# Performance work log

Measured on AMD Instinct MI355X. Metric: run time of the kernel, lower is better.

The kernel has to match this reference:

```python
import jax, jax.numpy as jnp
import numpy as np

B, N, K, C = 4, 4096, 32, 192  # batch, npoint, nsample, channels (C % 6 == 0)
EPS = 1e-5


def setup_inputs() -> dict:
    key = jax.random.key(0)
    ks = jax.random.split(key, 8)
    p = jax.random.normal(ks[0], (B, N, 3), jnp.float32)
    x = jax.random.normal(ks[1], (B, C, N), jnp.float32)
    idx = jax.random.randint(ks[2], (B, N, K), 0, N)  # ball-query neighbor ids
    W = jax.random.normal(ks[3], (C, C + 3), jnp.float32) * 0.05  # 1x1 conv weight
    gamma = 1.0 + 0.1 * jax.random.normal(ks[4], (C,), jnp.float32)
    beta = 0.1 * jax.random.normal(ks[5], (C,), jnp.float32)
    rmean = 0.1 * jax.random.normal(ks[6], (C,), jnp.float32)
    rvar = jax.random.uniform(ks[7], (C,), jnp.float32) + 0.5  # positive running var
    return dict(p=p, x=x, idx=idx, W=W, gamma=gamma, beta=beta, rmean=rmean, rvar=rvar)


def reference(p, x, idx, W, gamma, beta, rmean, rvar):
    # --- grouper: gather neighbors, relative coords ---
    pn = jax.vmap(lambda pp, ii: pp[ii])(p, idx)            # [B,N,K,3]
    dp = jnp.transpose(pn - p[:, :, None, :], (0, 3, 1, 2))  # [B,3,N,K]
    xj = jax.vmap(lambda xx, ii: xx[:, ii])(x, idx)          # [B,C,N,K]
    # --- PosPool sin/cos positional embedding fused with features ---
    feat_dim = C // 6
    dim_mat = jnp.power(500.0, jnp.arange(feat_dim, dtype=jnp.float32) / feat_dim)
    div = (50.0 * dp)[..., None] / dim_mat                   # [B,3,N,K,fd]
    pe = jnp.concatenate([jnp.sin(div), jnp.cos(div)], axis=-1)  # [B,3,N,K,2fd]
    pe = jnp.transpose(pe, (0, 1, 4, 2, 3)).reshape(B, C, N, K)  # [B,C,N,K]
    agg = xj * pe + pe
    # --- dp_fj concat -> 1x1 conv -> BN(eval) -> ReLU ---
    h = jnp.concatenate([dp, agg], axis=1)                   # [B,C+3,N,K]
    y = jnp.einsum('oc,bcnk->bonk', W, h)                    # [B,C,N,K]
    inv = gamma / jnp.sqrt(rvar + EPS)
    y = y * inv[:, None, None] + (beta - rmean * inv)[:, None, None]
    y = jax.nn.relu(y)
    # --- max reduction over neighbors ---
    return jnp.max(y, axis=-1)                               # [B,C,N]
```

## Files before the change

### kernel.cpp

```cpp
#include <hip/hip_runtime.h>
#include <math.h>

#define B_   4
#define N_   4096
#define K_   32
#define C_   192
#define CH_  195
#define KPAD 224
#define NKT  7
#define NNT  4
#define NPAIR (B_ * N_ / 2)
#define GRID  768

using half8  = __attribute__((ext_vector_type(8))) _Float16;
using half2v = __attribute__((ext_vector_type(2))) _Float16;
using f32x4  = __attribute__((ext_vector_type(4))) float;

__device__ _Float16 g_Wp[C_ * KPAD];
__device__ _Float16 g_xT[(size_t)B_ * N_ * C_];

__global__ __launch_bounds__(256) void prep(const float* __restrict__ x,
                                            const float* __restrict__ W,
                                            const float* __restrict__ gamma_,
                                            const float* __restrict__ rvar) {
    const int tid = threadIdx.x;
    if (blockIdx.x < 512) {
        __shared__ float s[32][201];
        const int b  = blockIdx.x >> 7;
        const int n0 = (blockIdx.x & 127) * 32;
        const int cl = tid >> 3;
        const int n4 = (tid & 7) * 4;
#pragma unroll
        for (int it = 0; it < 6; ++it) {
            const int c = it * 32 + cl;
            const float4 v = *(const float4*)(x + ((size_t)b * C_ + c) * N_ + n0 + n4);
            s[n4 + 0][c] = v.x; s[n4 + 1][c] = v.y; s[n4 + 2][c] = v.z; s[n4 + 3][c] = v.w;
        }
        __syncthreads();
        const int n  = tid >> 3;
        const int og = tid & 7;
#pragma unroll
        for (int it = 0; it < 3; ++it) {
            const int oc = it * 8 + og;
            half8 v;
#pragma unroll
            for (int jj = 0; jj < 8; ++jj) v[jj] = (_Float16)s[n][oc * 8 + jj];
            *(half8*)(g_xT + ((size_t)b * N_ + n0 + n) * C_ + oc * 8) = v;
        }
    } else {
        const int i = (blockIdx.x - 512) * 256 + tid;
        if (i < C_ * KPAD) {
            const int o = i / KPAD, r = i - o * KPAD;
            const float inv = gamma_[o] * rsqrtf(rvar[o] + 1e-5f);
            float v = 0.0f;
            if (r < 192)      v = W[o * CH_ + 3 + r];
            else if (r < 195) v = W[o * CH_ + (r - 192)];
            g_Wp[i] = (_Float16)(v * inv);
        }
    }
}

__global__ __launch_bounds__(256, 3) void la_mfma(
    const float* __restrict__ p,
    const int*   __restrict__ idx,
    const float* __restrict__ gamma_,
    const float* __restrict__ beta_,
    const float* __restrict__ rmean,
    const float* __restrict__ rvar,
    float* __restrict__ out)
{
    __shared__ _Float16 hb[NKT * NNT * 64 * 8];
    __shared__ float s_bias[C_], s_fr[32], s_out[C_ * 2];

    const int tid  = threadIdx.x;
    const int lane = tid & 63;
    const int w    = tid >> 6;
    const int l15  = lane & 15;
    const int quad = lane >> 4;

    const int xcd    = blockIdx.x & 7;
    const int slot   = blockIdx.x >> 3;
    const int st     = (slot < 64) ? slot * 11 : slot * 10 + 64;
    const int npairs = (slot < 64) ? 11 : 10;
    const int pair0  = xcd * 1024 + st;
    const int b      = xcd >> 1;

    if (tid < C_) {
        const float inv = gamma_[tid] * rsqrtf(rvar[tid] + 1e-5f);
        s_bias[tid] = beta_[tid] - rmean[tid] * inv;
    }
    if (tid < 32) s_fr[tid] = 7.9577471546f * exp2f(-(float)tid * 0.2801808715263400f);
    __syncthreads();

    float sfr[8];
#pragma unroll
    for (int jj = 0; jj < 8; ++jj) sfr[jj] = s_fr[quad * 8 + jj];

    half8 wf[3][NKT];
#pragma unroll
    for (int i = 0; i < 3; ++i)
#pragma unroll
        for (int kt = 0; kt < NKT; ++kt)
            wf[i][kt] = *(const half8*)(g_Wp + (size_t)((w * 3 + i) * 16 + l15) * KPAD
                                              + kt * 32 + quad * 8);

    const int pt = w >> 1;
    const int k  = (w & 1) * 16 + l15;

    int j = idx[(size_t)(pair0 * 2 + pt) * K_ + k];

    for (int it = 0; it < npairs; ++it) {
        const int bn0 = (pair0 + it) * 2;
        const int n0  = bn0 & (N_ - 1);
        const int gp  = bn0 + pt;

        const float d0 = p[(size_t)(b * N_ + j) * 3 + 0] - p[(size_t)gp * 3 + 0];
        const float d1 = p[(size_t)(b * N_ + j) * 3 + 1] - p[(size_t)gp * 3 + 1];
        const float d2 = p[(size_t)(b * N_ + j) * 3 + 2] - p[(size_t)gp * 3 + 2];
        const _Float16* xh = g_xT + ((size_t)b * N_ + j) * C_;

#pragma unroll
        for (int i6 = 0; i6 < 6; ++i6) {
            const int chunk = quad + 4 * i6;
            const half8 v = *(const half8*)(xh + chunk * 8);
            const float dd  = (chunk < 8) ? d0 : ((chunk < 16) ? d1 : d2);
            const float off = (chunk & 4) ? 0.25f : 0.0f;
            half8 hv;
#pragma unroll
            for (int jj = 0; jj < 8; jj += 2) {
                const float pe0 = __builtin_amdgcn_sinf(fmaf(dd, sfr[jj],     off));
                const float pe1 = __builtin_amdgcn_sinf(fmaf(dd, sfr[jj + 1], off));
                const half2v pe2 = __builtin_bit_cast(half2v, __builtin_amdgcn_cvt_pkrtz(pe0, pe1));
                half2v v2; v2[0] = v[jj]; v2[1] = v[jj + 1];
                const half2v r2 = pe2 * v2 + pe2;
                hv[jj] = r2[0]; hv[jj + 1] = r2[1];
            }
            const int kt = chunk >> 2;
            *(half8*)(&hb[(size_t)((kt * NNT + w) * 64 + quad * 16 + l15) * 8]) = hv;
        }
        if (quad == 0) {
            half8 hv0 = (half8)(_Float16)0.0f;
            hv0[0] = (_Float16)d0; hv0[1] = (_Float16)d1; hv0[2] = (_Float16)d2;
            *(half8*)(&hb[(size_t)((6 * NNT + w) * 64 + 0 * 16 + l15) * 8]) = hv0;
        } else {
            *(half8*)(&hb[(size_t)((6 * NNT + w) * 64 + quad * 16 + l15) * 8]) = (half8)(_Float16)0.0f;
        }
        __syncthreads();

        {
            const int itn = (it + 1 < npairs) ? it + 1 : it;
            j = idx[(size_t)((pair0 + itn) * 2 + pt) * K_ + k];
        }

        f32x4 acc[3][4];
#pragma unroll
        for (int i = 0; i < 3; ++i)
#pragma unroll
            for (int t = 0; t < 4; ++t) acc[i][t] = (f32x4)0.0f;

#pragma unroll
        for (int kt = 0; kt < NKT; ++kt) {
            half8 bf[4];
#pragma unroll
            for (int t = 0; t < 4; ++t)
                bf[t] = *(const half8*)(&hb[(size_t)((kt * NNT + t) * 64 + lane) * 8]);
#pragma unroll
            for (int i = 0; i < 3; ++i)
#pragma unroll
                for (int t = 0; t < 4; ++t)
                    acc[i][t] = __builtin_amdgcn_mfma_f32_16x16x32_f16(bf[t], wf[i][kt], acc[i][t], 0, 0, 0);
        }

#pragma unroll
        for (int i = 0; i < 3; ++i) {
            const int m = (w * 3 + i) * 16 + l15;
            float vv[2];
#pragma unroll
            for (int ptc = 0; ptc < 2; ++ptc) {
                const f32x4 va = acc[i][2 * ptc];
                const f32x4 vb = acc[i][2 * ptc + 1];
                float v = fmaxf(fmaxf(fmaxf(va[0], va[1]), fmaxf(va[2], va[3])),
                                fmaxf(fmaxf(vb[0], vb[1]), fmaxf(vb[2], vb[3])));
                v = fmaxf(v, __shfl_xor(v, 16, 64));
                v = fmaxf(v, __shfl_xor(v, 32, 64));
                vv[ptc] = v;
            }
            if (quad == 0) {
                const float bias = s_bias[m];
                float2 o2;
                o2.x = fmaxf(vv[0] + bias, 0.0f);
                o2.y = fmaxf(vv[1] + bias, 0.0f);
                *(float2*)(&s_out[m * 2]) = o2;
            }
        }
        __syncthreads();

        if (tid < C_) {
            const float2 o2 = *(const float2*)(&s_out[tid * 2]);
            *(float2*)(&out[((size_t)b * C_ + tid) * N_ + n0]) = o2;
        }
    }
}

extern "C" void kernel_launch(void* const* d_in, const int* in_sizes, int n_in,
                              void* d_out, int out_size, void* d_ws, size_t ws_size,
                              hipStream_t stream) {
    (void)in_sizes; (void)n_in; (void)out_size; (void)d_ws; (void)ws_size;
    const float* p      = (const float*)d_in[0];
    const float* x      = (const float*)d_in[1];
    const int*   idx    = (const int*)d_in[2];
    const float* W      = (const float*)d_in[3];
    const float* gamma_ = (const float*)d_in[4];
    const float* beta_  = (const float*)d_in[5];
    const float* rmean  = (const float*)d_in[6];
    const float* rvar   = (const float*)d_in[7];
    float* out = (float*)d_out;

    prep<<<512 + (C_ * KPAD + 255) / 256, 256, 0, stream>>>(x, W, gamma_, rvar);
    la_mfma<<<GRID, 256, 0, stream>>>(p, idx, gamma_, beta_, rmean, rvar, out);
}
```

Baseline: 173.2 us.

## Prefetch next pair's gathered features into registers and stream weights from global

Software-pipelines the neighbour gather. The next iteration's idx, point coordinates and 48 fp16 feature values per lane are loaded into registers during the current MFMA phase, so gather latency is hidden behind compute. To free registers for this, the 21 half8 weight fragments held for the whole kernel are dropped and reloaded from global memory (mostly L2/L1 hits) in each k-tile. The trade is extra weight-load traffic and latency inside the MFMA loop in exchange for overlapping the dependent gather loads.

```diff
diff --git a/kernel.cpp b/kernel.cpp
--- a/kernel.cpp
+++ b/kernel.cpp
@@ -9,8 +9,7 @@
 #define KPAD 224
 #define NKT  7
 #define NNT  4
-#define NPAIR (B_ * N_ / 2)
-#define GRID  768
+#define GRID 768
 
 using half8  = __attribute__((ext_vector_type(8))) _Float16;
 using half2v = __attribute__((ext_vector_type(2))) _Float16;
@@ -96,33 +95,41 @@
 #pragma unroll
     for (int jj = 0; jj < 8; ++jj) sfr[jj] = s_fr[quad * 8 + jj];
 
-    half8 wf[3][NKT];
-#pragma unroll
-    for (int i = 0; i < 3; ++i)
-#pragma unroll
-        for (int kt = 0; kt < NKT; ++kt)
-            wf[i][kt] = *(const half8*)(g_Wp + (size_t)((w * 3 + i) * 16 + l15) * KPAD
-                                              + kt * 32 + quad * 8);
-
     const int pt = w >> 1;
     const int k  = (w & 1) * 16 + l15;
 
-    int j = idx[(size_t)(pair0 * 2 + pt) * K_ + k];
+    float px0, px1, px2;
+    float pj0, pj1, pj2;
+    half8 xh[6];
+    {
+        const int gp0 = pair0 * 2 + pt;
+        const int j0  = idx[(size_t)gp0 * K_ + k];
+        px0 = p[(size_t)gp0 * 3 + 0]; px1 = p[(size_t)gp0 * 3 + 1]; px2 = p[(size_t)gp0 * 3 + 2];
+        pj0 = p[(size_t)(b * N_ + j0) * 3 + 0];
+        pj1 = p[(size_t)(b * N_ + j0) * 3 + 1];
+        pj2 = p[(size_t)(b * N_ + j0) * 3 + 2];
+        const _Float16* xh0 = g_xT + ((size_t)b * N_ + j0) * C_;
+#pragma unroll
+        for (int i6 = 0; i6 < 6; ++i6) xh[i6] = *(const half8*)(xh0 + (quad + 4 * i6) * 8);
+    }
 
     for (int it = 0; it < npairs; ++it) {
         const int bn0 = (pair0 + it) * 2;
         const int n0  = bn0 & (N_ - 1);
-        const int gp  = bn0 + pt;
-
-        const float d0 = p[(size_t)(b * N_ + j) * 3 + 0] - p[(size_t)gp * 3 + 0];
-        const float d1 = p[(size_t)(b * N_ + j) * 3 + 1] - p[(size_t)gp * 3 + 1];
-        const float d2 = p[(size_t)(b * N_ + j) * 3 + 2] - p[(size_t)gp * 3 + 2];
-        const _Float16* xh = g_xT + ((size_t)b * N_ + j) * C_;
+
+        const int itn = (it + 1 < npairs) ? it + 1 : it;
+        const int gpn = (pair0 + itn) * 2 + pt;
+        const int j_next = idx[(size_t)gpn * K_ + k];
+        const float pxn0 = p[(size_t)gpn * 3 + 0];
+        const float pxn1 = p[(size_t)gpn * 3 + 1];
+        const float pxn2 = p[(size_t)gpn * 3 + 2];
+
+        const float d0 = pj0 - px0, d1 = pj1 - px1, d2 = pj2 - px2;
 
 #pragma unroll
         for (int i6 = 0; i6 < 6; ++i6) {
             const int chunk = quad + 4 * i6;
-            const half8 v = *(const half8*)(xh + chunk * 8);
+            const half8 v = xh[i6];
             const float dd  = (chunk < 8) ? d0 : ((chunk < 16) ? d1 : d2);
             const float off = (chunk & 4) ? 0.25f : 0.0f;
             half8 hv;
@@ -147,9 +154,15 @@
         }
         __syncthreads();
 
+        float pjn0, pjn1, pjn2;
+        half8 xhn[6];
         {
-            const int itn = (it + 1 < npairs) ? it + 1 : it;
-            j = idx[(size_t)((pair0 + itn) * 2 + pt) * K_ + k];
+            pjn0 = p[(size_t)(b * N_ + j_next) * 3 + 0];
+            pjn1 = p[(size_t)(b * N_ + j_next) * 3 + 1];
+            pjn2 = p[(size_t)(b * N_ + j_next) * 3 + 2];
+            const _Float16* xhp = g_xT + ((size_t)b * N_ + j_next) * C_;
+#pragma unroll
+            for (int i6 = 0; i6 < 6; ++i6) xhn[i6] = *(const half8*)(xhp + (quad + 4 * i6) * 8);
         }
 
         f32x4 acc[3][4];
@@ -160,7 +173,11 @@
 
 #pragma unroll
         for (int kt = 0; kt < NKT; ++kt) {
-            half8 bf[4];
+            const int k0 = kt * 32 + quad * 8;
+            half8 a[3], bf[4];
+#pragma unroll
+            for (int i = 0; i < 3; ++i)
+                a[i] = *(const half8*)(g_Wp + (size_t)((w * 3 + i) * 16 + l15) * KPAD + k0);
 #pragma unroll
             for (int t = 0; t < 4; ++t)
                 bf[t] = *(const half8*)(&hb[(size_t)((kt * NNT + t) * 64 + lane) * 8]);
@@ -168,7 +185,7 @@
             for (int i = 0; i < 3; ++i)
 #pragma unroll
                 for (int t = 0; t < 4; ++t)
-                    acc[i][t] = __builtin_amdgcn_mfma_f32_16x16x32_f16(bf[t], wf[i][kt], acc[i][t], 0, 0, 0);
+                    acc[i][t] = __builtin_amdgcn_mfma_f32_16x16x32_f16(bf[t], a[i], acc[i][t], 0, 0, 0);
         }
 
 #pragma unroll
@@ -199,6 +216,11 @@
             const float2 o2 = *(const float2*)(&s_out[tid * 2]);
             *(float2*)(&out[((size_t)b * C_ + tid) * N_ + n0]) = o2;
         }
+
+        px0 = pxn0; px1 = pxn1; px2 = pxn2;
+        pj0 = pjn0; pj1 = pjn1; pj2 = pjn2;
+#pragma unroll
+        for (int i6 = 0; i6 < 6; ++i6) xh[i6] = xhn[i6];
     }
 }
 
```

Measured after the change: 169.3 us. 2.3% less time.

## Stream weights from global per k-tile, double-buffer LDS, drop second barrier

Applied to the files above, without the earlier changes.

Weight fragments are no longer held in registers for the whole kernel. They are reloaded from global (L2-resident) memory inside each k-tile loop, which frees a large block of VGPRs. The LDS feature buffer is double-buffered so the trailing output barrier can be removed, and results go straight to global memory from the quad-0 lanes. The dp tile is rebuilt from a small LDS array rather than a zero-padded half8 tile. The cost is repeated global weight loads on the MFMA critical path and scattered 8-byte output stores.

```diff
diff --git a/kernel.cpp b/kernel.cpp
--- a/kernel.cpp
+++ b/kernel.cpp
@@ -7,10 +7,9 @@
 #define C_   192
 #define CH_  195
 #define KPAD 224
-#define NKT  7
+#define NKT6 6
 #define NNT  4
-#define NPAIR (B_ * N_ / 2)
-#define GRID  768
+#define GRID 768
 
 using half8  = __attribute__((ext_vector_type(8))) _Float16;
 using half2v = __attribute__((ext_vector_type(2))) _Float16;
@@ -69,8 +68,9 @@
     const float* __restrict__ rvar,
     float* __restrict__ out)
 {
-    __shared__ _Float16 hb[NKT * NNT * 64 * 8];
-    __shared__ float s_bias[C_], s_fr[32], s_out[C_ * 2];
+    __shared__ _Float16 hb[2][NKT6 * NNT * 64 * 8];
+    __shared__ float s_d[2][3][64];
+    __shared__ float s_bias[C_], s_fr[32];
 
     const int tid  = threadIdx.x;
     const int lane = tid & 63;
@@ -96,20 +96,13 @@
 #pragma unroll
     for (int jj = 0; jj < 8; ++jj) sfr[jj] = s_fr[quad * 8 + jj];
 
-    half8 wf[3][NKT];
-#pragma unroll
-    for (int i = 0; i < 3; ++i)
-#pragma unroll
-        for (int kt = 0; kt < NKT; ++kt)
-            wf[i][kt] = *(const half8*)(g_Wp + (size_t)((w * 3 + i) * 16 + l15) * KPAD
-                                              + kt * 32 + quad * 8);
-
     const int pt = w >> 1;
     const int k  = (w & 1) * 16 + l15;
 
     int j = idx[(size_t)(pair0 * 2 + pt) * K_ + k];
 
     for (int it = 0; it < npairs; ++it) {
+        const int cur = it & 1;
         const int bn0 = (pair0 + it) * 2;
         const int n0  = bn0 & (N_ - 1);
         const int gp  = bn0 + pt;
@@ -135,15 +128,11 @@
                 const half2v r2 = pe2 * v2 + pe2;
                 hv[jj] = r2[0]; hv[jj + 1] = r2[1];
             }
-            const int kt = chunk >> 2;
-            *(half8*)(&hb[(size_t)((kt * NNT + w) * 64 + quad * 16 + l15) * 8]) = hv;
+            *(half8*)(&hb[cur][(size_t)((i6 * NNT + w) * 64 + quad * 16 + l15) * 8]) = hv;
         }
         if (quad == 0) {
-            half8 hv0 = (half8)(_Float16)0.0f;
-            hv0[0] = (_Float16)d0; hv0[1] = (_Float16)d1; hv0[2] = (_Float16)d2;
-            *(half8*)(&hb[(size_t)((6 * NNT + w) * 64 + 0 * 16 + l15) * 8]) = hv0;
-        } else {
-            *(half8*)(&hb[(size_t)((6 * NNT + w) * 64 + quad * 16 + l15) * 8]) = (half8)(_Float16)0.0f;
+            const int col = w * 16 + l15;
+            s_d[cur][0][col] = d0; s_d[cur][1][col] = d1; s_d[cur][2][col] = d2;
         }
         __syncthreads();
 
@@ -159,16 +148,40 @@
             for (int t = 0; t < 4; ++t) acc[i][t] = (f32x4)0.0f;
 
 #pragma unroll
-        for (int kt = 0; kt < NKT; ++kt) {
-            half8 bf[4];
+        for (int kt = 0; kt < NKT6; ++kt) {
+            const int k0 = kt * 32 + quad * 8;
+            half8 a[3], bf[4];
+#pragma unroll
+            for (int i = 0; i < 3; ++i)
+                a[i] = *(const half8*)(g_Wp + (size_t)((w * 3 + i) * 16 + l15) * KPAD + k0);
 #pragma unroll
             for (int t = 0; t < 4; ++t)
-                bf[t] = *(const half8*)(&hb[(size_t)((kt * NNT + t) * 64 + lane) * 8]);
+                bf[t] = *(const half8*)(&hb[cur][(size_t)((kt * NNT + t) * 64 + lane) * 8]);
 #pragma unroll
             for (int i = 0; i < 3; ++i)
 #pragma unroll
                 for (int t = 0; t < 4; ++t)
-                    acc[i][t] = __builtin_amdgcn_mfma_f32_16x16x32_f16(bf[t], wf[i][kt], acc[i][t], 0, 0, 0);
+                    acc[i][t] = __builtin_amdgcn_mfma_f32_16x16x32_f16(bf[t], a[i], acc[i][t], 0, 0, 0);
+        }
+        {
+            half8 a6[3];
+#pragma unroll
+            for (int i = 0; i < 3; ++i)
+                a6[i] = *(const half8*)(g_Wp + (size_t)((w * 3 + i) * 16 + l15) * KPAD + 6 * 32 + quad * 8);
+#pragma unroll
+            for (int t = 0; t < 4; ++t) {
+                const int col = t * 16 + l15;
+                half8 b6 = (half8)(_Float16)0.0f;
+                const float e0 = s_d[cur][0][col];
+                const float e1 = s_d[cur][1][col];
+                const float e2 = s_d[cur][2][col];
+                if (quad == 0) {
+                    b6[0] = (_Float16)e0; b6[1] = (_Float16)e1; b6[2] = (_Float16)e2;
+                }
+#pragma unroll
+                for (int i = 0; i < 3; ++i)
+                    acc[i][t] = __builtin_amdgcn_mfma_f32_16x16x32_f16(b6, a6[i], acc[i][t], 0, 0, 0);
+            }
         }
 
 #pragma unroll
@@ -190,14 +203,8 @@
                 float2 o2;
                 o2.x = fmaxf(vv[0] + bias, 0.0f);
                 o2.y = fmaxf(vv[1] + bias, 0.0f);
-                *(float2*)(&s_out[m * 2]) = o2;
-            }
-        }
-        __syncthreads();
-
-        if (tid < C_) {
-            const float2 o2 = *(const float2*)(&s_out[tid * 2]);
-            *(float2*)(&out[((size_t)b * C_ + tid) * N_ + n0]) = o2;
+                *(float2*)(&out[((size_t)b * C_ + m) * N_ + n0]) = o2;
+            }
         }
     }
 }
```

Measured after the change: 158.4 us. 1.09x faster.
